# Kernel optimization log

Measured on AMD Instinct MI355X. Metric: run time of the kernel, lower is better.

## Reference

```python
import jax, jax.numpy as jnp
import numpy as np

ALPHA = 8.3  # depth-similarity sharpness from the Depth-aware CNN paper
K = 3        # kernel size
PAD = 1      # padding (stride=1, dilation=1)


def setup_inputs() -> dict:
    key = jax.random.key(0)
    k1, k2, k3, k4 = jax.random.split(key, 4)
    B, Cin, Cout, H, W = 8, 128, 128, 128, 128
    inp = {
        "input": jax.random.normal(k1, (B, Cin, H, W), dtype=jnp.float32),
        "depth": jax.random.uniform(k2, (B, 1, H, W), dtype=jnp.float32),
        "weight": jax.random.normal(k3, (Cout, Cin, K, K), dtype=jnp.float32) * 0.05,
        "bias": jax.random.normal(k4, (Cout,), dtype=jnp.float32) * 0.05,
    }
    return inp


def reference(input, depth, weight, bias):
    # Depth-aware convolution: out(b,o,y,x) = sum_{c,kh,kw} W(o,c,kh,kw)
    #   * x(b,c,y+kh-1,x+kw-1) * exp(-ALPHA * |D(b,y,x) - D(b,y+kh-1,x+kw-1)|)
    # stride=1, dilation=1, padding=1 -> output spatial == input spatial.
    B, C, H, W = input.shape
    xp = jnp.pad(input, ((0, 0), (0, 0), (PAD, PAD), (PAD, PAD)))
    dp = jnp.pad(depth, ((0, 0), (0, 0), (PAD, PAD), (PAD, PAD)))
    acc = jnp.zeros((B, weight.shape[0], H, W), dtype=input.dtype)
    for kh in range(K):
        for kw in range(K):
            xs = xp[:, :, kh:kh + H, kw:kw + W]          # [B,C,H,W] shifted window
            ds = dp[:, :, kh:kh + H, kw:kw + W]          # [B,1,H,W]
            sim = jnp.exp(-ALPHA * jnp.abs(depth - ds))  # [B,1,H,W]
            acc = acc + jnp.einsum('bchw,oc->bohw', xs * sim, weight[:, :, kh, kw])
    return acc + bias[None, :, None, None]
```

## Files before the change

kernel.cpp:

```cpp
#include <hip/hip_runtime.h>
#include <hip/hip_bf16.h>
#include <cstdint>

#define ALPHA 8.3f

typedef __attribute__((ext_vector_type(8))) short bf16x8;
typedef __attribute__((ext_vector_type(4))) float f32x4;
typedef unsigned int u32;

__device__ __align__(16) short g_wt[9 * 128 * 128];
__device__ __align__(16) short g_xt[(size_t)8 * 130 * 130 * 128];
__device__ float g_dp[8 * 130 * 130];

__device__ __forceinline__ short f2bf(float f) {
    union { float f; uint32_t u; } v; v.f = f;
    uint32_t r = v.u + 0x7fffu + ((v.u >> 16) & 1u);
    return (short)(r >> 16);
}

__global__ __launch_bounds__(256) void prep(const float* __restrict__ w,
                                            const float* __restrict__ depth) {
    int idx = blockIdx.x * 256 + threadIdx.x;
    if (idx < 147456) {
        int c = idx & 127, o = (idx >> 7) & 127, tap = idx >> 14;
        g_wt[idx] = f2bf(w[(o * 128 + c) * 9 + tap]);
    } else if (idx < 147456 + 135200) {
        int u = idx - 147456;
        int b = u / 16900; int rem = u - b * 16900;
        int hp = rem / 130, wp = rem - hp * 130;
        float v = 0.f;
        if (hp >= 1 && hp <= 128 && wp >= 1 && wp <= 128)
            v = depth[b * 16384 + (hp - 1) * 128 + (wp - 1)];
        g_dp[u] = v;
    } else if (idx < 147456 + 135200 + 66048) {
        int u = idx - (147456 + 135200);
        int b = u / 8256; int rem = u - b * 8256;
        int pos = rem >> 4, unit = rem & 15;
        int hp, wp;
        if (pos < 130)      { hp = 0;         wp = pos; }
        else if (pos < 260) { hp = 129;       wp = pos - 130; }
        else if (pos < 388) { hp = pos - 259; wp = 0; }
        else                { hp = pos - 387; wp = 129; }
        size_t off = (((size_t)b * 130 + hp) * 130 + wp) * 128 + unit * 8;
        *reinterpret_cast<bf16x8*>(g_xt + off) = (bf16x8){0,0,0,0,0,0,0,0};
    }
}

__global__ __launch_bounds__(256) void x_transpose(const float* __restrict__ x) {
    __shared__ __align__(16) short T[128 * 128];
    const int b = blockIdx.x >> 7;
    const int h = blockIdx.x & 127;
    const int tid = threadIdx.x;
    char* tp = (char*)T;

    const int w = tid & 127;
    const int c0 = tid >> 7;
    const float* xb = x + (size_t)b * (128 * 16384) + h * 128 + w;
    #pragma unroll
    for (int i = 0; i < 64; ++i) {
        int c = c0 + i * 2;
        float v = xb[(size_t)c * 16384];
        int byte = (w << 8) | ((c << 1) ^ ((w & 15) << 4));
        *reinterpret_cast<short*>(tp + byte) = f2bf(v);
    }
    __syncthreads();

    size_t obase = (((size_t)b * 130 + h + 1) * 130 + 1) * 128;
    #pragma unroll
    for (int iter = 0; iter < 8; ++iter) {
        int idx = tid + iter * 256;
        int oct = idx & 15;
        int ww = idx >> 4;
        int byte = (ww << 8) | ((oct << 4) ^ ((ww & 15) << 4));
        bf16x8 v = *reinterpret_cast<const bf16x8*>(tp + byte);
        *reinterpret_cast<bf16x8*>(g_xt + obase + (size_t)ww * 128 + oct * 8) = v;
    }
}

__global__ __launch_bounds__(256, 2) void depthconv_main(
    const float* __restrict__ bias, float* __restrict__ out)
{
    __shared__ __align__(16) short Xs[264 * 128];
    __shared__ float simL[9][2][64];

    const int blk = blockIdx.x;
    const int b = blk >> 7;
    const int rem = blk & 127;
    const int h0 = (rem >> 1) << 1;
    const int w0 = (rem & 1) << 6;

    const int tid = threadIdx.x;
    const int lane = tid & 63;
    const int wid = tid >> 6;
    char* xsp = (char*)Xs;

    const char* xtb = (const char*)g_xt +
        (((size_t)b * 130 + h0) * 130 + w0) * 256;
    #pragma unroll
    for (int iter = 0; iter < 17; ++iter) {
        int it = tid + iter * 256;
        if (it < 4224) {
            int row = it >> 4;
            int c16 = (it & 15) ^ (row & 15);
            int r4 = row / 66;
            int wl = row - r4 * 66;
            const char* src = xtb + ((size_t)(r4 * 130 + wl)) * 256 + (c16 << 4);
            __builtin_amdgcn_global_load_lds(
                (const __attribute__((address_space(1))) u32*)src,
                (__attribute__((address_space(3))) u32*)(xsp + it * 16),
                16, 0, 0);
        }
    }

    const float* dpb = g_dp + b * 16900;
    #pragma unroll
    for (int iter = 0; iter < 5; ++iter) {
        int idx = tid + iter * 256;
        if (idx < 1152) {
            int t = idx >> 7;
            int r2 = idx & 127;
            int hsel = r2 >> 6;
            int wo = r2 & 63;
            int kh = t / 3, kw = t - 3 * kh;
            int ho = h0 + hsel;
            float dc  = dpb[(ho + 1) * 130 + w0 + wo + 1];
            float dsv = dpb[(ho + kh) * 130 + w0 + wo + kw];
            simL[t][hsel][wo] = __expf(-ALPHA * fabsf(dc - dsv));
        }
    }
    __syncthreads();

    const int l15 = lane & 15;
    const int khi = lane >> 4;
    const int wo2 = wid & 1;
    const int hsel = wid >> 1;
    const int obase = wo2 << 6;

    f32x4 acc[4][4];
    #pragma unroll
    for (int i = 0; i < 4; ++i)
        #pragma unroll
        for (int j = 0; j < 4; ++j)
            acc[i][j] = (f32x4){0.f, 0.f, 0.f, 0.f};

    #pragma unroll
    for (int r = 0; r < 3; ++r) {
        #pragma unroll
        for (int kw = 0; kw < 3; ++kw) {
            const int tap = r * 3 + kw;
            const short* wtap = g_wt + tap * 16384;

            float sim[4];
            #pragma unroll
            for (int j = 0; j < 4; ++j)
                sim[j] = simL[tap][hsel][j * 16 + l15];

            f32x4 P[4][4];
            #pragma unroll
            for (int i = 0; i < 4; ++i)
                #pragma unroll
                for (int j = 0; j < 4; ++j)
                    P[i][j] = (f32x4){0.f, 0.f, 0.f, 0.f};

            #pragma unroll
            for (int ks = 0; ks < 4; ++ks) {
                const int cb = ks * 32 + (khi << 3);
                bf16x8 afr[4], bfr[4];
                #pragma unroll
                for (int i = 0; i < 4; ++i)
                    afr[i] = *reinterpret_cast<const bf16x8*>(
                        wtap + (obase + i * 16 + l15) * 128 + cb);
                #pragma unroll
                for (int j = 0; j < 4; ++j) {
                    int row = (hsel + r) * 66 + j * 16 + l15 + kw;
                    int byte = (row << 8) | ((cb << 1) ^ ((row & 15) << 4));
                    bfr[j] = *reinterpret_cast<const bf16x8*>(xsp + byte);
                }
                #pragma unroll
                for (int i = 0; i < 4; ++i)
                    #pragma unroll
                    for (int j = 0; j < 4; ++j)
                        P[i][j] = __builtin_amdgcn_mfma_f32_16x16x32_bf16(
                            afr[i], bfr[j], P[i][j], 0, 0, 0);
            }

            #pragma unroll
            for (int j = 0; j < 4; ++j) {
                float sv = sim[j];
                #pragma unroll
                for (int i = 0; i < 4; ++i)
                    #pragma unroll
                    for (int rr = 0; rr < 4; ++rr)
                        acc[i][j][rr] += sv * P[i][j][rr];
            }
        }
    }

    #pragma unroll
    for (int i = 0; i < 4; ++i) {
        #pragma unroll
        for (int rr = 0; rr < 4; ++rr) {
            const int o = obase + i * 16 + (khi << 2) + rr;
            const float bv = bias[o];
            float* orow = out + (((size_t)(b * 128 + o)) * 128 + (h0 + hsel)) * 128 + w0;
            #pragma unroll
            for (int j = 0; j < 4; ++j)
                orow[j * 16 + l15] = acc[i][j][rr] + bv;
        }
    }
}

extern "C" void kernel_launch(void* const* d_in, const int* in_sizes, int n_in,
                              void* d_out, int out_size, void* d_ws, size_t ws_size,
                              hipStream_t stream) {
    const float* x     = (const float*)d_in[0];
    const float* depth = (const float*)d_in[1];
    const float* wgt   = (const float*)d_in[2];
    const float* bias  = (const float*)d_in[3];
    float* out = (float*)d_out;

    hipLaunchKernelGGL(prep, dim3(1363), dim3(256), 0, stream, wgt, depth);
    hipLaunchKernelGGL(x_transpose, dim3(8 * 128), dim3(256), 0, stream, x);
    hipLaunchKernelGGL(depthconv_main, dim3(8 * 64 * 2), dim3(256), 0, stream,
                       bias, out);
}
```

Before: 205.4 us.

## Split main tile across 8 waves, prefetch weights into registers, re-layout x buffer

The main kernel now runs 512 threads, with each wave computing a 64x32 output sub-tile instead of 64x64. Weight fragments are held in registers and prefetched for the next half-K or tap ahead of the MFMAs, which removes redundant per-iteration global weight loads. The padded x buffer moves to a [b][h][c16][w][8] layout, and the transpose kernel stages fp32 in padded shared memory before packing to bf16. This targets latency hiding and occupancy, but fewer MFMAs per fragment load lowers register-level reuse of the shared-memory B operands, and the new layout changes the gather pattern.

After: 450.5 us. 2.19x slower.

```diff
diff --git a/kernel.cpp b/kernel.cpp
--- a/kernel.cpp
+++ b/kernel.cpp
@@ -9,13 +9,17 @@
 typedef unsigned int u32;
 
 __device__ __align__(16) short g_wt[9 * 128 * 128];
-__device__ __align__(16) short g_xt[(size_t)8 * 130 * 130 * 128];
+__device__ __align__(16) short g_xt[(size_t)8 * 130 * 16 * 130 * 8];
 __device__ float g_dp[8 * 130 * 130];
 
 __device__ __forceinline__ short f2bf(float f) {
     union { float f; uint32_t u; } v; v.f = f;
     uint32_t r = v.u + 0x7fffu + ((v.u >> 16) & 1u);
     return (short)(r >> 16);
+}
+
+__device__ __forceinline__ size_t xt_off(int b, int hp, int c16, int wp) {
+    return ((((size_t)b * 130 + hp) * 16 + c16) * 130 + wp) * 8;
 }
 
 __global__ __launch_bounds__(256) void prep(const float* __restrict__ w,
@@ -41,43 +45,37 @@
         else if (pos < 260) { hp = 129;       wp = pos - 130; }
         else if (pos < 388) { hp = pos - 259; wp = 0; }
         else                { hp = pos - 387; wp = 129; }
-        size_t off = (((size_t)b * 130 + hp) * 130 + wp) * 128 + unit * 8;
-        *reinterpret_cast<bf16x8*>(g_xt + off) = (bf16x8){0,0,0,0,0,0,0,0};
+        *reinterpret_cast<bf16x8*>(g_xt + xt_off(b, hp, unit, wp)) =
+            (bf16x8){0, 0, 0, 0, 0, 0, 0, 0};
     }
 }
 
 __global__ __launch_bounds__(256) void x_transpose(const float* __restrict__ x) {
-    __shared__ __align__(16) short T[128 * 128];
+    __shared__ float T[128 * 129];
     const int b = blockIdx.x >> 7;
     const int h = blockIdx.x & 127;
     const int tid = threadIdx.x;
-    char* tp = (char*)T;
-
     const int w = tid & 127;
-    const int c0 = tid >> 7;
-    const float* xb = x + (size_t)b * (128 * 16384) + h * 128 + w;
-    #pragma unroll
-    for (int i = 0; i < 64; ++i) {
-        int c = c0 + i * 2;
-        float v = xb[(size_t)c * 16384];
-        int byte = (w << 8) | ((c << 1) ^ ((w & 15) << 4));
-        *reinterpret_cast<short*>(tp + byte) = f2bf(v);
-    }
+    const int ch = tid >> 7;
+
+    const float* xb = x + ((size_t)(b * 128 + ch * 64)) * 16384 + h * 128 + w;
+    #pragma unroll
+    for (int k = 0; k < 64; ++k)
+        T[w * 129 + ch * 64 + k] = xb[(size_t)k * 16384];
     __syncthreads();
 
-    size_t obase = (((size_t)b * 130 + h + 1) * 130 + 1) * 128;
-    #pragma unroll
-    for (int iter = 0; iter < 8; ++iter) {
-        int idx = tid + iter * 256;
-        int oct = idx & 15;
-        int ww = idx >> 4;
-        int byte = (ww << 8) | ((oct << 4) ^ ((ww & 15) << 4));
-        bf16x8 v = *reinterpret_cast<const bf16x8*>(tp + byte);
-        *reinterpret_cast<bf16x8*>(g_xt + obase + (size_t)ww * 128 + oct * 8) = v;
-    }
-}
-
-__global__ __launch_bounds__(256, 2) void depthconv_main(
+    #pragma unroll
+    for (int k = 0; k < 8; ++k) {
+        int c16 = ch * 8 + k;
+        const float* tr = T + w * 129 + c16 * 8;
+        bf16x8 pk;
+        #pragma unroll
+        for (int i = 0; i < 8; ++i) pk[i] = f2bf(tr[i]);
+        *reinterpret_cast<bf16x8*>(g_xt + xt_off(b, h + 1, c16, w + 1)) = pk;
+    }
+}
+
+__global__ __launch_bounds__(512, 4) void depthconv_main(
     const float* __restrict__ bias, float* __restrict__ out)
 {
     __shared__ __align__(16) short Xs[264 * 128];
@@ -92,19 +90,34 @@
     const int tid = threadIdx.x;
     const int lane = tid & 63;
     const int wid = tid >> 6;
+    const int hsel = wid >> 2;
+    const int ohalf = (wid >> 1) & 1;
+    const int wq = wid & 1;
+    const int l15 = lane & 15;
+    const int khi = lane >> 4;
+    const int obase = ohalf << 6;
     char* xsp = (char*)Xs;
 
-    const char* xtb = (const char*)g_xt +
-        (((size_t)b * 130 + h0) * 130 + w0) * 256;
-    #pragma unroll
-    for (int iter = 0; iter < 17; ++iter) {
-        int it = tid + iter * 256;
+    const short* wlane = g_wt + (obase + l15) * 128 + khi * 8;
+
+    bf16x8 wreg[8];
+    #pragma unroll
+    for (int i = 0; i < 4; ++i)
+        #pragma unroll
+        for (int kk = 0; kk < 2; ++kk)
+            wreg[i * 2 + kk] =
+                *reinterpret_cast<const bf16x8*>(wlane + i * 2048 + kk * 32);
+
+    #pragma unroll
+    for (int iter = 0; iter < 9; ++iter) {
+        int it = tid + iter * 512;
         if (it < 4224) {
             int row = it >> 4;
-            int c16 = (it & 15) ^ (row & 15);
+            int u = it & 15;
             int r4 = row / 66;
             int wl = row - r4 * 66;
-            const char* src = xtb + ((size_t)(r4 * 130 + wl)) * 256 + (c16 << 4);
+            int c16 = u ^ (row & 15);
+            const short* src = g_xt + xt_off(b, h0 + r4, c16, w0 + wl);
             __builtin_amdgcn_global_load_lds(
                 (const __attribute__((address_space(1))) u32*)src,
                 (__attribute__((address_space(3))) u32*)(xsp + it * 16),
@@ -114,86 +127,86 @@
 
     const float* dpb = g_dp + b * 16900;
     #pragma unroll
-    for (int iter = 0; iter < 5; ++iter) {
-        int idx = tid + iter * 256;
+    for (int iter = 0; iter < 3; ++iter) {
+        int idx = tid + iter * 512;
         if (idx < 1152) {
             int t = idx >> 7;
             int r2 = idx & 127;
-            int hsel = r2 >> 6;
+            int hs = r2 >> 6;
             int wo = r2 & 63;
-            int kh = t / 3, kw = t - 3 * kh;
-            int ho = h0 + hsel;
+            int kh = t / 3, kw2 = t - 3 * kh;
+            int ho = h0 + hs;
             float dc  = dpb[(ho + 1) * 130 + w0 + wo + 1];
-            float dsv = dpb[(ho + kh) * 130 + w0 + wo + kw];
-            simL[t][hsel][wo] = __expf(-ALPHA * fabsf(dc - dsv));
+            float dsv = dpb[(ho + kh) * 130 + w0 + wo + kw2];
+            simL[t][hs][wo] = __expf(-ALPHA * fabsf(dc - dsv));
         }
     }
     __syncthreads();
 
-    const int l15 = lane & 15;
-    const int khi = lane >> 4;
-    const int wo2 = wid & 1;
-    const int hsel = wid >> 1;
-    const int obase = wo2 << 6;
-
-    f32x4 acc[4][4];
+    f32x4 acc[4][2];
     #pragma unroll
     for (int i = 0; i < 4; ++i)
         #pragma unroll
-        for (int j = 0; j < 4; ++j)
+        for (int j = 0; j < 2; ++j)
             acc[i][j] = (f32x4){0.f, 0.f, 0.f, 0.f};
 
-    #pragma unroll
-    for (int r = 0; r < 3; ++r) {
-        #pragma unroll
-        for (int kw = 0; kw < 3; ++kw) {
-            const int tap = r * 3 + kw;
-            const short* wtap = g_wt + tap * 16384;
-
-            float sim[4];
+    const f32x4 z4 = (f32x4){0.f, 0.f, 0.f, 0.f};
+
+    #pragma unroll
+    for (int tap = 0; tap < 9; ++tap) {
+        const int r = tap / 3;
+        const int kw = tap - 3 * r;
+        const int rowb = (hsel + r) * 66 + wq * 32 + l15 + kw;
+
+        f32x4 P[4][2];
+
+        #pragma unroll
+        for (int half = 0; half < 2; ++half) {
             #pragma unroll
-            for (int j = 0; j < 4; ++j)
-                sim[j] = simL[tap][hsel][j * 16 + l15];
-
-            f32x4 P[4][4];
-            #pragma unroll
-            for (int i = 0; i < 4; ++i)
-                #pragma unroll
-                for (int j = 0; j < 4; ++j)
-                    P[i][j] = (f32x4){0.f, 0.f, 0.f, 0.f};
-
-            #pragma unroll
-            for (int ks = 0; ks < 4; ++ks) {
-                const int cb = ks * 32 + (khi << 3);
-                bf16x8 afr[4], bfr[4];
-                #pragma unroll
-                for (int i = 0; i < 4; ++i)
-                    afr[i] = *reinterpret_cast<const bf16x8*>(
-                        wtap + (obase + i * 16 + l15) * 128 + cb);
-                #pragma unroll
-                for (int j = 0; j < 4; ++j) {
-                    int row = (hsel + r) * 66 + j * 16 + l15 + kw;
+            for (int kk = 0; kk < 2; ++kk) {
+                const int ks = half * 2 + kk;
+                const int cb = ks * 32 + khi * 8;
+                bf16x8 bfr[2];
+                #pragma unroll
+                for (int j = 0; j < 2; ++j) {
+                    int row = rowb + j * 16;
                     int byte = (row << 8) | ((cb << 1) ^ ((row & 15) << 4));
                     bfr[j] = *reinterpret_cast<const bf16x8*>(xsp + byte);
                 }
                 #pragma unroll
                 for (int i = 0; i < 4; ++i)
                     #pragma unroll
-                    for (int j = 0; j < 4; ++j)
+                    for (int j = 0; j < 2; ++j)
                         P[i][j] = __builtin_amdgcn_mfma_f32_16x16x32_bf16(
-                            afr[i], bfr[j], P[i][j], 0, 0, 0);
+                            wreg[i * 2 + kk], bfr[j],
+                            (half == 0 && kk == 0) ? z4 : P[i][j], 0, 0, 0);
             }
-
-            #pragma unroll
-            for (int j = 0; j < 4; ++j) {
-                float sv = sim[j];
+            if (half == 0) {
                 #pragma unroll
                 for (int i = 0; i < 4; ++i)
                     #pragma unroll
-                    for (int rr = 0; rr < 4; ++rr)
-                        acc[i][j][rr] += sv * P[i][j][rr];
+                    for (int kk = 0; kk < 2; ++kk)
+                        wreg[i * 2 + kk] = *reinterpret_cast<const bf16x8*>(
+                            wlane + tap * 16384 + i * 2048 + 64 + kk * 32);
+            } else if (tap < 8) {
+                #pragma unroll
+                for (int i = 0; i < 4; ++i)
+                    #pragma unroll
+                    for (int kk = 0; kk < 2; ++kk)
+                        wreg[i * 2 + kk] = *reinterpret_cast<const bf16x8*>(
+                            wlane + (tap + 1) * 16384 + i * 2048 + kk * 32);
             }
         }
+
+        float sv0 = simL[tap][hsel][wq * 32 + l15];
+        float sv1 = simL[tap][hsel][wq * 32 + 16 + l15];
+        #pragma unroll
+        for (int i = 0; i < 4; ++i)
+            #pragma unroll
+            for (int rr = 0; rr < 4; ++rr) {
+                acc[i][0][rr] += sv0 * P[i][0][rr];
+                acc[i][1][rr] += sv1 * P[i][1][rr];
+            }
     }
 
     #pragma unroll
@@ -202,10 +215,10 @@
         for (int rr = 0; rr < 4; ++rr) {
             const int o = obase + i * 16 + (khi << 2) + rr;
             const float bv = bias[o];
-            float* orow = out + (((size_t)(b * 128 + o)) * 128 + (h0 + hsel)) * 128 + w0;
-            #pragma unroll
-            for (int j = 0; j < 4; ++j)
-                orow[j * 16 + l15] = acc[i][j][rr] + bv;
+            float* orow = out + (((size_t)(b * 128 + o)) * 128 + (h0 + hsel)) * 128
+                          + w0 + wq * 32;
+            orow[l15] = acc[i][0][rr] + bv;
+            orow[16 + l15] = acc[i][1][rr] + bv;
         }
     }
 }
@@ -221,6 +234,6 @@
 
     hipLaunchKernelGGL(prep, dim3(1363), dim3(256), 0, stream, wgt, depth);
     hipLaunchKernelGGL(x_transpose, dim3(8 * 128), dim3(256), 0, stream, x);
-    hipLaunchKernelGGL(depthconv_main, dim3(8 * 64 * 2), dim3(256), 0, stream,
+    hipLaunchKernelGGL(depthconv_main, dim3(8 * 64 * 2), dim3(512), 0, stream,
                        bias, out);
 }
```
